# Optimization experiments

Hardware: AMD Instinct MI355X
Metric: run time of the kernel (lower is better)

The kernel has to match this reference:

```python
import jax, jax.numpy as jnp
import numpy as np

SCALE = 0.08838834764831845  # 1/sqrt(128)


def setup_inputs() -> dict:
    key = jax.random.key(0)
    k1, k2, k3, k4 = jax.random.split(key, 4)
    B, Sq, H, D = 1, 2048, 32, 128
    Skv, K = 4096, 256
    return {
        "q": jax.random.normal(k1, (B, Sq, H, D), jnp.float32),
        "kv": jax.random.normal(k2, (B, Skv, 2, D), jnp.float32),  # stacked K,V (MQA)
        "attn_sink": jax.random.normal(k3, (H,), jnp.float32),
        "topk_idxs": jax.random.randint(k4, (B, Sq, K), 0, Skv),
    }


def reference(q, kv, attn_sink, topk_idxs):
    # q:        [B, Sq, H, D]
    # kv:       [B, Skv, 2, D]  (index 0 = keys, 1 = values; shared across heads)
    # topk_idxs:[B, Sq, K]      per-query selected KV positions
    # attn_sink:[H]             per-head sink logit added to the softmax denominator
    B = q.shape[0]
    # Gather selected KV per query: [B, Sq, K, 2, D]
    gathered = kv[jnp.arange(B)[:, None, None], topk_idxs]
    k = gathered[..., 0, :]  # [B, Sq, K, D]
    v = gathered[..., 1, :]  # [B, Sq, K, D]

    scores = jnp.einsum("bqhd,bqkd->bqhk", q, k) * SCALE  # [B, Sq, H, K]
    sink = attn_sink[None, None, :, None]                  # [1, 1, H, 1]

    # Numerically stable softmax over K selected tokens + sink logit.
    m = jnp.maximum(jnp.max(scores, axis=-1, keepdims=True), sink)
    e = jnp.exp(scores - m)
    denom = jnp.sum(e, axis=-1, keepdims=True) + jnp.exp(sink - m)
    probs = e / denom                                      # sink absorbs leftover mass

    out = jnp.einsum("bqhk,bqkd->bqhd", probs, v)          # [B, Sq, H, D]
    return out
```

## Files before the change

kernel.cpp:

```cpp
#include <hip/hip_runtime.h>
#include <hip/hip_bf16.h>

#define SQ 2048
#define NH 32
#define DH 128
#define NK 256
#define SCALE 0.08838834764831845f
#define LOG2E 1.4426950408889634f

typedef __attribute__((ext_vector_type(8))) __bf16 bf16x8;
typedef __attribute__((ext_vector_type(4))) float floatx4;

#define KS_STRIDE 136
#define VB_STRIDE 72
#define PB_STRIDE 264

#define OFF_KV   16896
#define OFF_RED  35328
#define OFF_RED2 35840
#define SMEM_SZ  36352

#define SCHED_PIN() __builtin_amdgcn_sched_barrier(0)

__device__ __forceinline__ unsigned pk_bf16(float a, float b) {
  union { __hip_bfloat162 h2; unsigned u; } c;
  c.h2 = __float22bfloat162_rn(make_float2(a, b));
  return c.u;
}

__device__ __forceinline__ float fast_exp2(float x) {
#if __has_builtin(__builtin_amdgcn_exp2f)
  return __builtin_amdgcn_exp2f(x);
#else
  return exp2f(x);
#endif
}

template <int CTRL>
__device__ __forceinline__ float dpp_rot(float x) {
  int i = __builtin_bit_cast(int, x);
  i = __builtin_amdgcn_mov_dpp(i, CTRL, 0xF, 0xF, true);
  return __builtin_bit_cast(float, i);
}
#define RED16_MAX(v) { v = fmaxf(v, dpp_rot<0x121>(v)); v = fmaxf(v, dpp_rot<0x122>(v)); \
                       v = fmaxf(v, dpp_rot<0x124>(v)); v = fmaxf(v, dpp_rot<0x128>(v)); }
#define RED16_SUM(v) { v += dpp_rot<0x121>(v); v += dpp_rot<0x122>(v); \
                       v += dpp_rot<0x124>(v); v += dpp_rot<0x128>(v); }

__global__ __launch_bounds__(256) void kv_to_bf16(const float* __restrict__ kv,
                                                  unsigned short* __restrict__ kvb) {
  int i = blockIdx.x * 256 + threadIdx.x;
  float4 f = ((const float4*)kv)[i];
  uint2 o = { pk_bf16(f.x, f.y), pk_bf16(f.z, f.w) };
  ((uint2*)kvb)[i] = o;
}

struct KR { uint4 v[4]; };
struct VR { uint4 a, b, c, d; };

__device__ __forceinline__ KR k_load(const unsigned short* __restrict__ kvb,
                                     const int* __restrict__ tkg, int c, int tid) {
  int r = tid >> 2, seg = tid & 3;
  int idx = tkg[c * 64 + r];
  const uint4* p = (const uint4*)(kvb + (size_t)idx * 256 + seg * 32);
  KR k;
#pragma unroll
  for (int i = 0; i < 4; i++) k.v[i] = p[i];
  return k;
}

__device__ __forceinline__ void k_write(unsigned short* kvbuf, const KR& k, int tid) {
  int r = tid >> 2, seg = tid & 3;
  uint4* d = (uint4*)&kvbuf[r * KS_STRIDE + seg * 32];
#pragma unroll
  for (int i = 0; i < 4; i++) d[i] = k.v[i];
}

__device__ __forceinline__ VR v_load(const unsigned short* __restrict__ kvb,
                                     const int* __restrict__ tkg, int c, int tid) {
  int rg = tid & 15, dg = tid >> 4;
  int r0 = rg * 4, d0 = dg * 8;
  int4 i4 = *(const int4*)&tkg[c * 64 + r0];
  VR v;
  v.a = *(const uint4*)(kvb + (size_t)i4.x * 256 + 128 + d0);
  v.b = *(const uint4*)(kvb + (size_t)i4.y * 256 + 128 + d0);
  v.c = *(const uint4*)(kvb + (size_t)i4.z * 256 + 128 + d0);
  v.d = *(const uint4*)(kvb + (size_t)i4.w * 256 + 128 + d0);
  return v;
}

__device__ __forceinline__ void v_write(unsigned short* kvbuf, const VR& v, int tid) {
  int rg = tid & 15, dg = tid >> 4;
  int r0 = rg * 4, d0 = dg * 8;
  const unsigned* pa = (const unsigned*)&v.a;
  const unsigned* pb = (const unsigned*)&v.b;
  const unsigned* pc = (const unsigned*)&v.c;
  const unsigned* pd = (const unsigned*)&v.d;
#pragma unroll
  for (int w = 0; w < 4; w++) {
    unsigned lo01 = __builtin_amdgcn_perm(pb[w], pa[w], 0x05040100u);
    unsigned lo23 = __builtin_amdgcn_perm(pd[w], pc[w], 0x05040100u);
    unsigned hi01 = __builtin_amdgcn_perm(pb[w], pa[w], 0x07060302u);
    unsigned hi23 = __builtin_amdgcn_perm(pd[w], pc[w], 0x07060302u);
    uint2 lo = { lo01, lo23 }, hi = { hi01, hi23 };
    *(uint2*)&kvbuf[(d0 + 2 * w) * VB_STRIDE + r0] = lo;
    *(uint2*)&kvbuf[(d0 + 2 * w + 1) * VB_STRIDE + r0] = hi;
  }
}

__device__ __forceinline__ void gemm1(const unsigned short* kvbuf,
                                      const bf16x8 af[2][4], int nrow, int quad,
                                      floatx4& a0, floatx4& a1) {
  a0 = (floatx4){0.f, 0.f, 0.f, 0.f};
  a1 = (floatx4){0.f, 0.f, 0.f, 0.f};
  __builtin_amdgcn_s_setprio(1);
#pragma unroll
  for (int ks = 0; ks < 4; ks++) {
    bf16x8 b = *(const bf16x8*)&kvbuf[nrow * KS_STRIDE + ks * 32 + quad * 8];
    a0 = __builtin_amdgcn_mfma_f32_16x16x32_bf16(af[0][ks], b, a0, 0, 0, 0);
    a1 = __builtin_amdgcn_mfma_f32_16x16x32_bf16(af[1][ks], b, a1, 0, 0, 0);
  }
  __builtin_amdgcn_s_setprio(0);
}

__device__ __forceinline__ void pv_chunk(const unsigned short* pbuf,
                                         const unsigned short* kvbuf, int c,
                                         int wave, int quad, int l16,
                                         floatx4 oacc[2][2]) {
  __builtin_amdgcn_s_setprio(1);
#pragma unroll
  for (int ks = 0; ks < 2; ks++) {
    int kof = c * 64 + ks * 32 + quad * 8;
    bf16x8 a0 = *(const bf16x8*)&pbuf[l16 * PB_STRIDE + kof];
    bf16x8 a1 = *(const bf16x8*)&pbuf[(16 + l16) * PB_STRIDE + kof];
    int kl = ks * 32 + quad * 8;
    bf16x8 b0 = *(const bf16x8*)&kvbuf[(wave * 32 + l16) * VB_STRIDE + kl];
    bf16x8 b1 = *(const bf16x8*)&kvbuf[(wave * 32 + 16 + l16) * VB_STRIDE + kl];
    oacc[0][0] = __builtin_amdgcn_mfma_f32_16x16x32_bf16(a0, b0, oacc[0][0], 0, 0, 0);
    oacc[0][1] = __builtin_amdgcn_mfma_f32_16x16x32_bf16(a0, b1, oacc[0][1], 0, 0, 0);
    oacc[1][0] = __builtin_amdgcn_mfma_f32_16x16x32_bf16(a1, b0, oacc[1][0], 0, 0, 0);
    oacc[1][1] = __builtin_amdgcn_mfma_f32_16x16x32_bf16(a1, b1, oacc[1][1], 0, 0, 0);
  }
  __builtin_amdgcn_s_setprio(0);
}

__global__ __launch_bounds__(256, 4) void sparse_attn_kernel(
    const float* __restrict__ q, const unsigned short* __restrict__ kvb,
    const float* __restrict__ sink, const int* __restrict__ topk,
    float* __restrict__ out) {
  __shared__ __align__(16) char smem[SMEM_SZ];
  unsigned short* pbuf  = (unsigned short*)smem;
  unsigned short* kvbuf = (unsigned short*)(smem + OFF_KV);
  float* red  = (float*)(smem + OFF_RED);
  float* red2 = (float*)(smem + OFF_RED2);

  const int tid = threadIdx.x;
  const int s = blockIdx.x;
  const int wave = tid >> 6;
  const int lane = tid & 63;
  const int quad = lane >> 4;
  const int l16 = lane & 15;
  const int* tkg = topk + (size_t)s * NK;

  KR k0 = k_load(kvb, tkg, 0, tid);
  SCHED_PIN();

  const float QSC = SCALE * LOG2E;
  const float* qp = q + (size_t)s * (NH * DH);
  float4 qf[2][4][2];
#pragma unroll
  for (int mt = 0; mt < 2; mt++)
#pragma unroll
    for (int ks = 0; ks < 4; ks++) {
      const float* base = qp + (mt * 16 + l16) * DH + ks * 32 + quad * 8;
      qf[mt][ks][0] = ((const float4*)base)[0];
      qf[mt][ks][1] = ((const float4*)base)[1];
    }
  KR k1 = k_load(kvb, tkg, 1, tid);
  KR k2 = k_load(kvb, tkg, 2, tid);
  SCHED_PIN();

  float snk[2][4];
#pragma unroll
  for (int mt = 0; mt < 2; mt++)
#pragma unroll
    for (int r = 0; r < 4; r++)
      snk[mt][r] = sink[mt * 16 + quad * 4 + r] * LOG2E;

  bf16x8 afrag[2][4];
#pragma unroll
  for (int mt = 0; mt < 2; mt++)
#pragma unroll
    for (int ks = 0; ks < 4; ks++) {
      float4 f0 = qf[mt][ks][0], f1 = qf[mt][ks][1];
      uint4 u = { pk_bf16(f0.x * QSC, f0.y * QSC), pk_bf16(f0.z * QSC, f0.w * QSC),
                  pk_bf16(f1.x * QSC, f1.y * QSC), pk_bf16(f1.z * QSC, f1.w * QSC) };
      afrag[mt][ks] = __builtin_bit_cast(bf16x8, u);
    }
  k_write(kvbuf, k0, tid);
  __syncthreads();

  const int nrow = wave * 16 + l16;

  floatx4 sc[4][2];
  gemm1(kvbuf, afrag, nrow, quad, sc[0][0], sc[0][1]);
  __syncthreads();
  k_write(kvbuf, k1, tid);
  KR k3 = k_load(kvb, tkg, 3, tid);
  SCHED_PIN();
  __syncthreads();

  gemm1(kvbuf, afrag, nrow, quad, sc[1][0], sc[1][1]);
  __syncthreads();
  k_write(kvbuf, k2, tid);
  VR v0 = v_load(kvb, tkg, 0, tid);
  SCHED_PIN();
  __syncthreads();

  gemm1(kvbuf, afrag, nrow, quad, sc[2][0], sc[2][1]);
  __syncthreads();
  k_write(kvbuf, k3, tid);
  VR v1 = v_load(kvb, tkg, 1, tid);
  SCHED_PIN();
  __syncthreads();

  gemm1(kvbuf, afrag, nrow, quad, sc[3][0], sc[3][1]);
  __syncthreads();
  v_write(kvbuf, v0, tid);

  float mh[2][4];
#pragma unroll
  for (int mt = 0; mt < 2; mt++)
#pragma unroll
    for (int r = 0; r < 4; r++) {
      float v = fmaxf(fmaxf(sc[0][mt][r], sc[1][mt][r]),
                      fmaxf(sc[2][mt][r], sc[3][mt][r]));
      RED16_MAX(v);
      mh[mt][r] = v;
    }
  if (l16 == 0) {
#pragma unroll
    for (int mt = 0; mt < 2; mt++)
#pragma unroll
      for (int r = 0; r < 4; r++)
        red[wave * 32 + mt * 16 + quad * 4 + r] = mh[mt][r];
  }
  __syncthreads();
  VR v2 = v_load(kvb, tkg, 2, tid);
  SCHED_PIN();
#pragma unroll
  for (int mt = 0; mt < 2; mt++)
#pragma unroll
    for (int r = 0; r < 4; r++) {
      int h = mt * 16 + quad * 4 + r;
      float v = snk[mt][r];
#pragma unroll
      for (int w = 0; w < 4; w++) v = fmaxf(v, red[w * 32 + h]);
      mh[mt][r] = v;
    }
  float ps[2][4];
#pragma unroll
  for (int mt = 0; mt < 2; mt++)
#pragma unroll
    for (int r = 0; r < 4; r++) {
      float acc = 0.f;
#pragma unroll
      for (int c = 0; c < 4; c++) {
        float e = fast_exp2(sc[c][mt][r] - mh[mt][r]);
        sc[c][mt][r] = e;
        acc += e;
      }
      RED16_SUM(acc);
      ps[mt][r] = acc;
    }
  if (l16 == 0) {
#pragma unroll
    for (int mt = 0; mt < 2; mt++)
#pragma unroll
      for (int r = 0; r < 4; r++)
        red2[wave * 32 + mt * 16 + quad * 4 + r] = ps[mt][r];
  }
  __syncthreads();
  float inv[2][4];
#pragma unroll
  for (int mt = 0; mt < 2; mt++)
#pragma unroll
    for (int r = 0; r < 4; r++) {
      float dd = fast_exp2(snk[mt][r] - mh[mt][r]);
#pragma unroll
      for (int w = 0; w < 4; w++) dd += red2[w * 32 + mt * 16 + quad * 4 + r];
      inv[mt][r] = 1.0f / dd;
    }
#pragma unroll
  for (int c = 0; c < 4; c++)
#pragma unroll
    for (int mt = 0; mt < 2; mt++) {
      int col = c * 64 + wave * 16 + l16;
      unsigned short* pb = &pbuf[(mt * 16 + quad * 4) * PB_STRIDE + col];
      unsigned p01 = pk_bf16(sc[c][mt][0], sc[c][mt][1]);
      unsigned p23 = pk_bf16(sc[c][mt][2], sc[c][mt][3]);
      pb[0] = (unsigned short)p01;
      pb[PB_STRIDE] = (unsigned short)(p01 >> 16);
      pb[2 * PB_STRIDE] = (unsigned short)p23;
      pb[3 * PB_STRIDE] = (unsigned short)(p23 >> 16);
    }
  __syncthreads();

  floatx4 oacc[2][2];
#pragma unroll
  for (int mt = 0; mt < 2; mt++)
#pragma unroll
    for (int nt = 0; nt < 2; nt++)
      oacc[mt][nt] = (floatx4){0.f, 0.f, 0.f, 0.f};

  VR v3 = v_load(kvb, tkg, 3, tid);
  SCHED_PIN();
  pv_chunk(pbuf, kvbuf, 0, wave, quad, l16, oacc);
  __syncthreads();
  v_write(kvbuf, v1, tid);
  __syncthreads();

  pv_chunk(pbuf, kvbuf, 1, wave, quad, l16, oacc);
  __syncthreads();
  v_write(kvbuf, v2, tid);
  __syncthreads();

  pv_chunk(pbuf, kvbuf, 2, wave, quad, l16, oacc);
  __syncthreads();
  v_write(kvbuf, v3, tid);
  __syncthreads();

  pv_chunk(pbuf, kvbuf, 3, wave, quad, l16, oacc);

  {
    float* op = out + (size_t)s * (NH * DH);
#pragma unroll
    for (int mt = 0; mt < 2; mt++)
#pragma unroll
      for (int nt = 0; nt < 2; nt++)
#pragma unroll
        for (int r4 = 0; r4 < 4; r4++) {
          int h = mt * 16 + quad * 4 + r4;
          int d = wave * 32 + nt * 16 + l16;
          op[h * DH + d] = oacc[mt][nt][r4] * inv[mt][r4];
        }
  }
}

extern "C" void kernel_launch(void* const* d_in, const int* in_sizes, int n_in,
                              void* d_out, int out_size, void* d_ws, size_t ws_size,
                              hipStream_t stream) {
  (void)in_sizes; (void)n_in; (void)out_size; (void)ws_size;
  const float* q    = (const float*)d_in[0];
  const float* kv   = (const float*)d_in[1];
  const float* sink = (const float*)d_in[2];
  const int*   topk = (const int*)d_in[3];
  float* out = (float*)d_out;
  unsigned short* kvb = (unsigned short*)d_ws;

  kv_to_bf16<<<dim3(1024), dim3(256), 0, stream>>>(kv, kvb);
  sparse_attn_kernel<<<dim3(SQ), dim3(256), 0, stream>>>(q, kvb, sink, topk, out);
}
```

Measured before the change: 129.1 us.

## Split heads across two blocks per query, swizzle LDS, merge softmax reductions

Measured after the change: 166.5 us. 29.0% more time.

```diff
diff --git a/kernel.cpp b/kernel.cpp
--- a/kernel.cpp
+++ b/kernel.cpp
@@ -11,16 +11,14 @@
 typedef __attribute__((ext_vector_type(8))) __bf16 bf16x8;
 typedef __attribute__((ext_vector_type(4))) float floatx4;
 
-#define KS_STRIDE 136
-#define VB_STRIDE 72
-#define PB_STRIDE 264
-
-#define OFF_KV   16896
-#define OFF_RED  35328
-#define OFF_RED2 35840
-#define SMEM_SZ  36352
+#define OFF_KV   8192
+#define OFF_RED  (OFF_KV + 16384)
+#define OFF_RED2 (OFF_RED + 256)
+#define SMEM_SZ  25088
 
 #define SCHED_PIN() __builtin_amdgcn_sched_barrier(0)
+
+__device__ __forceinline__ int swz(int row) { return ((row ^ (row >> 3)) & 7) << 4; }
 
 __device__ __forceinline__ unsigned pk_bf16(float a, float b) {
   union { __hip_bfloat162 h2; unsigned u; } c;
@@ -69,11 +67,13 @@
   return k;
 }
 
-__device__ __forceinline__ void k_write(unsigned short* kvbuf, const KR& k, int tid) {
+__device__ __forceinline__ void k_write(char* kbuf, const KR& k, int tid) {
   int r = tid >> 2, seg = tid & 3;
-  uint4* d = (uint4*)&kvbuf[r * KS_STRIDE + seg * 32];
-#pragma unroll
-  for (int i = 0; i < 4; i++) d[i] = k.v[i];
+  int base = r * 256 + seg * 64;
+  int sw = swz(r);
+#pragma unroll
+  for (int i = 0; i < 4; i++)
+    *(uint4*)(kbuf + ((base + i * 16) ^ sw)) = k.v[i];
 }
 
 __device__ __forceinline__ VR v_load(const unsigned short* __restrict__ kvb,
@@ -89,7 +89,7 @@
   return v;
 }
 
-__device__ __forceinline__ void v_write(unsigned short* kvbuf, const VR& v, int tid) {
+__device__ __forceinline__ void v_write(char* vbuf, const VR& v, int tid) {
   int rg = tid & 15, dg = tid >> 4;
   int r0 = rg * 4, d0 = dg * 8;
   const unsigned* pa = (const unsigned*)&v.a;
@@ -103,247 +103,209 @@
     unsigned hi01 = __builtin_amdgcn_perm(pb[w], pa[w], 0x07060302u);
     unsigned hi23 = __builtin_amdgcn_perm(pd[w], pc[w], 0x07060302u);
     uint2 lo = { lo01, lo23 }, hi = { hi01, hi23 };
-    *(uint2*)&kvbuf[(d0 + 2 * w) * VB_STRIDE + r0] = lo;
-    *(uint2*)&kvbuf[(d0 + 2 * w + 1) * VB_STRIDE + r0] = hi;
-  }
-}
-
-__device__ __forceinline__ void gemm1(const unsigned short* kvbuf,
-                                      const bf16x8 af[2][4], int nrow, int quad,
-                                      floatx4& a0, floatx4& a1) {
-  a0 = (floatx4){0.f, 0.f, 0.f, 0.f};
-  a1 = (floatx4){0.f, 0.f, 0.f, 0.f};
+    int ra = d0 + 2 * w, rb = ra + 1;
+    *(uint2*)(vbuf + ((ra * 128 + r0 * 2) ^ swz(ra))) = lo;
+    *(uint2*)(vbuf + ((rb * 128 + r0 * 2) ^ swz(rb))) = hi;
+  }
+}
+
+__device__ __forceinline__ void gemm1(const char* kbuf, const bf16x8 af[4],
+                                      int nrow, int quad, floatx4& acc) {
+  acc = (floatx4){0.f, 0.f, 0.f, 0.f};
+  int sw = swz(nrow);
   __builtin_amdgcn_s_setprio(1);
 #pragma unroll
   for (int ks = 0; ks < 4; ks++) {
-    bf16x8 b = *(const bf16x8*)&kvbuf[nrow * KS_STRIDE + ks * 32 + quad * 8];
-    a0 = __builtin_amdgcn_mfma_f32_16x16x32_bf16(af[0][ks], b, a0, 0, 0, 0);
-    a1 = __builtin_amdgcn_mfma_f32_16x16x32_bf16(af[1][ks], b, a1, 0, 0, 0);
+    bf16x8 b = *(const bf16x8*)(kbuf + ((nrow * 256 + ks * 64 + quad * 16) ^ sw));
+    acc = __builtin_amdgcn_mfma_f32_16x16x32_bf16(af[ks], b, acc, 0, 0, 0);
   }
   __builtin_amdgcn_s_setprio(0);
 }
 
-__device__ __forceinline__ void pv_chunk(const unsigned short* pbuf,
-                                         const unsigned short* kvbuf, int c,
+__device__ __forceinline__ void pv_chunk(const char* pbuf, const char* vbuf, int c,
                                          int wave, int quad, int l16,
-                                         floatx4 oacc[2][2]) {
+                                         floatx4 oacc[2]) {
   __builtin_amdgcn_s_setprio(1);
 #pragma unroll
   for (int ks = 0; ks < 2; ks++) {
-    int kof = c * 64 + ks * 32 + quad * 8;
-    bf16x8 a0 = *(const bf16x8*)&pbuf[l16 * PB_STRIDE + kof];
-    bf16x8 a1 = *(const bf16x8*)&pbuf[(16 + l16) * PB_STRIDE + kof];
-    int kl = ks * 32 + quad * 8;
-    bf16x8 b0 = *(const bf16x8*)&kvbuf[(wave * 32 + l16) * VB_STRIDE + kl];
-    bf16x8 b1 = *(const bf16x8*)&kvbuf[(wave * 32 + 16 + l16) * VB_STRIDE + kl];
-    oacc[0][0] = __builtin_amdgcn_mfma_f32_16x16x32_bf16(a0, b0, oacc[0][0], 0, 0, 0);
-    oacc[0][1] = __builtin_amdgcn_mfma_f32_16x16x32_bf16(a0, b1, oacc[0][1], 0, 0, 0);
-    oacc[1][0] = __builtin_amdgcn_mfma_f32_16x16x32_bf16(a1, b0, oacc[1][0], 0, 0, 0);
-    oacc[1][1] = __builtin_amdgcn_mfma_f32_16x16x32_bf16(a1, b1, oacc[1][1], 0, 0, 0);
+    int kof = (c * 64 + ks * 32 + quad * 8) * 2;
+    bf16x8 a = *(const bf16x8*)(pbuf + ((l16 * 512 + kof) ^ swz(l16)));
+    int kl = (ks * 32 + quad * 8) * 2;
+    int r0 = wave * 32 + l16, r1 = r0 + 16;
+    bf16x8 b0 = *(const bf16x8*)(vbuf + ((r0 * 128 + kl) ^ swz(r0)));
+    bf16x8 b1 = *(const bf16x8*)(vbuf + ((r1 * 128 + kl) ^ swz(r1)));
+    oacc[0] = __builtin_amdgcn_mfma_f32_16x16x32_bf16(a, b0, oacc[0], 0, 0, 0);
+    oacc[1] = __builtin_amdgcn_mfma_f32_16x16x32_bf16(a, b1, oacc[1], 0, 0, 0);
   }
   __builtin_amdgcn_s_setprio(0);
 }
 
-__global__ __launch_bounds__(256, 4) void sparse_attn_kernel(
+__global__ __launch_bounds__(256, 5) void sparse_attn_kernel(
     const float* __restrict__ q, const unsigned short* __restrict__ kvb,
     const float* __restrict__ sink, const int* __restrict__ topk,
     float* __restrict__ out) {
   __shared__ __align__(16) char smem[SMEM_SZ];
-  unsigned short* pbuf  = (unsigned short*)smem;
-  unsigned short* kvbuf = (unsigned short*)(smem + OFF_KV);
+  char* pbuf  = smem;
+  char* kvbuf = smem + OFF_KV;
   float* red  = (float*)(smem + OFF_RED);
   float* red2 = (float*)(smem + OFF_RED2);
 
   const int tid = threadIdx.x;
-  const int s = blockIdx.x;
+  const int s = blockIdx.x >> 1;
+  const int h0 = (blockIdx.x & 1) * 16;
   const int wave = tid >> 6;
   const int lane = tid & 63;
   const int quad = lane >> 4;
   const int l16 = lane & 15;
   const int* tkg = topk + (size_t)s * NK;
 
-  KR k0 = k_load(kvb, tkg, 0, tid);
-  SCHED_PIN();
+  {
+    int r = tid >> 2, seg = tid & 3;
+    int idx = tkg[r];
+    const uint4* p = (const uint4*)(kvb + (size_t)idx * 256 + seg * 32);
+    uint4 t0 = p[0], t1 = p[1], t2 = p[2], t3 = p[3];
+    int base = r * 256 + seg * 64, sw = swz(r);
+    *(uint4*)(kvbuf + ((base) ^ sw)) = t0;
+    *(uint4*)(kvbuf + ((base + 16) ^ sw)) = t1;
+    *(uint4*)(kvbuf + ((base + 32) ^ sw)) = t2;
+    *(uint4*)(kvbuf + ((base + 48) ^ sw)) = t3;
+  }
+  KR k1 = k_load(kvb, tkg, 1, tid);
+  SCHED_PIN();
+
+  float snk[4];
+#pragma unroll
+  for (int r = 0; r < 4; r++)
+    snk[r] = sink[h0 + quad * 4 + r] * LOG2E;
 
   const float QSC = SCALE * LOG2E;
-  const float* qp = q + (size_t)s * (NH * DH);
-  float4 qf[2][4][2];
-#pragma unroll
-  for (int mt = 0; mt < 2; mt++)
-#pragma unroll
-    for (int ks = 0; ks < 4; ks++) {
-      const float* base = qp + (mt * 16 + l16) * DH + ks * 32 + quad * 8;
-      qf[mt][ks][0] = ((const float4*)base)[0];
-      qf[mt][ks][1] = ((const float4*)base)[1];
+  const float* qrow = q + (size_t)s * (NH * DH) + (h0 + l16) * DH;
+  bf16x8 afrag[4];
+#pragma unroll
+  for (int ks = 0; ks < 4; ks++) {
+    const float* base = qrow + ks * 32 + quad * 8;
+    float4 f0 = ((const float4*)base)[0];
+    float4 f1 = ((const float4*)base)[1];
+    uint4 u = { pk_bf16(f0.x * QSC, f0.y * QSC), pk_bf16(f0.z * QSC, f0.w * QSC),
+                pk_bf16(f1.x * QSC, f1.y * QSC), pk_bf16(f1.z * QSC, f1.w * QSC) };
+    afrag[ks] = __builtin_bit_cast(bf16x8, u);
+  }
+  __syncthreads();
+
+  const int nrow = wave * 16 + l16;
+
+  floatx4 sc[4];
+  KR k2 = k_load(kvb, tkg, 2, tid);
+  SCHED_PIN();
+  gemm1(kvbuf, afrag, nrow, quad, sc[0]);
+  __syncthreads();
+  k_write(kvbuf, k1, tid);
+  __syncthreads();
+  KR k3 = k_load(kvb, tkg, 3, tid);
+  SCHED_PIN();
+  gemm1(kvbuf, afrag, nrow, quad, sc[1]);
+  __syncthreads();
+  k_write(kvbuf, k2, tid);
+  __syncthreads();
+  VR v0 = v_load(kvb, tkg, 0, tid);
+  SCHED_PIN();
+  gemm1(kvbuf, afrag, nrow, quad, sc[2]);
+  __syncthreads();
+  k_write(kvbuf, k3, tid);
+  __syncthreads();
+  VR v1 = v_load(kvb, tkg, 1, tid);
+  SCHED_PIN();
+  gemm1(kvbuf, afrag, nrow, quad, sc[3]);
+
+  float mh[4], ps[4];
+#pragma unroll
+  for (int r = 0; r < 4; r++) {
+    float v = fmaxf(fmaxf(sc[0][r], sc[1][r]), fmaxf(sc[2][r], sc[3][r]));
+    RED16_MAX(v);
+    mh[r] = v;
+  }
+#pragma unroll
+  for (int r = 0; r < 4; r++) {
+    float acc = 0.f;
+#pragma unroll
+    for (int c = 0; c < 4; c++) {
+      float e = fast_exp2(sc[c][r] - mh[r]);
+      sc[c][r] = e;
+      acc += e;
     }
-  KR k1 = k_load(kvb, tkg, 1, tid);
-  KR k2 = k_load(kvb, tkg, 2, tid);
-  SCHED_PIN();
-
-  float snk[2][4];
-#pragma unroll
-  for (int mt = 0; mt < 2; mt++)
-#pragma unroll
-    for (int r = 0; r < 4; r++)
-      snk[mt][r] = sink[mt * 16 + quad * 4 + r] * LOG2E;
-
-  bf16x8 afrag[2][4];
-#pragma unroll
-  for (int mt = 0; mt < 2; mt++)
-#pragma unroll
-    for (int ks = 0; ks < 4; ks++) {
-      float4 f0 = qf[mt][ks][0], f1 = qf[mt][ks][1];
-      uint4 u = { pk_bf16(f0.x * QSC, f0.y * QSC), pk_bf16(f0.z * QSC, f0.w * QSC),
-                  pk_bf16(f1.x * QSC, f1.y * QSC), pk_bf16(f1.z * QSC, f1.w * QSC) };
-      afrag[mt][ks] = __builtin_bit_cast(bf16x8, u);
+    RED16_SUM(acc);
+    ps[r] = acc;
+  }
+  if (l16 == 0) {
+#pragma unroll
+    for (int r = 0; r < 4; r++) {
+      red[wave * 16 + quad * 4 + r]  = mh[r];
+      red2[wave * 16 + quad * 4 + r] = ps[r];
     }
-  k_write(kvbuf, k0, tid);
-  __syncthreads();
-
-  const int nrow = wave * 16 + l16;
-
-  floatx4 sc[4][2];
-  gemm1(kvbuf, afrag, nrow, quad, sc[0][0], sc[0][1]);
-  __syncthreads();
-  k_write(kvbuf, k1, tid);
-  KR k3 = k_load(kvb, tkg, 3, tid);
-  SCHED_PIN();
-  __syncthreads();
-
-  gemm1(kvbuf, afrag, nrow, quad, sc[1][0], sc[1][1]);
-  __syncthreads();
-  k_write(kvbuf, k2, tid);
-  VR v0 = v_load(kvb, tkg, 0, tid);
-  SCHED_PIN();
-  __syncthreads();
-
-  gemm1(kvbuf, afrag, nrow, quad, sc[2][0], sc[2][1]);
-  __syncthreads();
-  k_write(kvbuf, k3, tid);
-  VR v1 = v_load(kvb, tkg, 1, tid);
-  SCHED_PIN();
-  __syncthreads();
-
-  gemm1(kvbuf, afrag, nrow, quad, sc[3][0], sc[3][1]);
+  }
   __syncthreads();
   v_write(kvbuf, v0, tid);
-
-  float mh[2][4];
-#pragma unroll
-  for (int mt = 0; mt < 2; mt++)
-#pragma unroll
-    for (int r = 0; r < 4; r++) {
-      float v = fmaxf(fmaxf(sc[0][mt][r], sc[1][mt][r]),
-                      fmaxf(sc[2][mt][r], sc[3][mt][r]));
-      RED16_MAX(v);
-      mh[mt][r] = v;
+  VR v2 = v_load(kvb, tkg, 2, tid);
+  SCHED_PIN();
+  float inv[4], sf[4];
+#pragma unroll
+  for (int r = 0; r < 4; r++) {
+    int h = quad * 4 + r;
+    float M = snk[r];
+#pragma unroll
+    for (int w = 0; w < 4; w++) M = fmaxf(M, red[w * 16 + h]);
+    float dd = fast_exp2(snk[r] - M);
+#pragma unroll
+    for (int w = 0; w < 4; w++)
+      dd += red2[w * 16 + h] * fast_exp2(red[w * 16 + h] - M);
+    inv[r] = 1.0f / dd;
+    sf[r] = fast_exp2(mh[r] - M);
+  }
+#pragma unroll
+  for (int c = 0; c < 4; c++) {
+    int col = c * 64 + wave * 16 + l16;
+    unsigned p01 = pk_bf16(sc[c][0] * sf[0], sc[c][1] * sf[1]);
+    unsigned p23 = pk_bf16(sc[c][2] * sf[2], sc[c][3] * sf[3]);
+    unsigned short vals[4] = { (unsigned short)p01, (unsigned short)(p01 >> 16),
+                               (unsigned short)p23, (unsigned short)(p23 >> 16) };
+#pragma unroll
+    for (int j = 0; j < 4; j++) {
+      int h = quad * 4 + j;
+      *(unsigned short*)(pbuf + ((h * 512 + col * 2) ^ swz(h))) = vals[j];
     }
-  if (l16 == 0) {
-#pragma unroll
-    for (int mt = 0; mt < 2; mt++)
-#pragma unroll
-      for (int r = 0; r < 4; r++)
-        red[wave * 32 + mt * 16 + quad * 4 + r] = mh[mt][r];
-  }
-  __syncthreads();
-  VR v2 = v_load(kvb, tkg, 2, tid);
-  SCHED_PIN();
-#pragma unroll
-  for (int mt = 0; mt < 2; mt++)
-#pragma unroll
-    for (int r = 0; r < 4; r++) {
-      int h = mt * 16 + quad * 4 + r;
-      float v = snk[mt][r];
-#pragma unroll
-      for (int w = 0; w < 4; w++) v = fmaxf(v, red[w * 32 + h]);
-      mh[mt][r] = v;
-    }
-  float ps[2][4];
-#pragma unroll
-  for (int mt = 0; mt < 2; mt++)
-#pragma unroll
-    for (int r = 0; r < 4; r++) {
-      float acc = 0.f;
-#pragma unroll
-      for (int c = 0; c < 4; c++) {
-        float e = fast_exp2(sc[c][mt][r] - mh[mt][r]);
-        sc[c][mt][r] = e;
-        acc += e;
+  }
+  __syncthreads();
+
+  floatx4 oacc[2];
+  oacc[0] = (floatx4){0.f, 0.f, 0.f, 0.f};
+  oacc[1] = (floatx4){0.f, 0.f, 0.f, 0.f};
+
+  VR v3 = v_load(kvb, tkg, 3, tid);
+  SCHED_PIN();
+  pv_chunk(pbuf, kvbuf, 0, wave, quad, l16, oacc);
+  __syncthreads();
+  v_write(kvbuf, v1, tid);
+  __syncthreads();
+  pv_chunk(pbuf, kvbuf, 1, wave, quad, l16, oacc);
+  __syncthreads();
+  v_write(kvbuf, v2, tid);
+  __syncthreads();
+  pv_chunk(pbuf, kvbuf, 2, wave, quad, l16, oacc);
+  __syncthreads();
+  v_write(kvbuf, v3, tid);
+  __syncthreads();
+  pv_chunk(pbuf, kvbuf, 3, wave, quad, l16, oacc);
+
+  {
+    float* op = out + (size_t)s * (NH * DH) + h0 * DH;
+#pragma unroll
+    for (int nt = 0; nt < 2; nt++)
+#pragma unroll
+      for (int r4 = 0; r4 < 4; r4++) {
+        int h = quad * 4 + r4;
+        int d = wave * 32 + nt * 16 + l16;
+        op[h * DH + d] = oacc[nt][r4] * inv[r4];
       }
-      RED16_SUM(acc);
-      ps[mt][r] = acc;
-    }
-  if (l16 == 0) {
-#pragma unroll
-    for (int mt = 0; mt < 2; mt++)
-#pragma unroll
-      for (int r = 0; r < 4; r++)
-        red2[wave * 32 + mt * 16 + quad * 4 + r] = ps[mt][r];
-  }
-  __syncthreads();
-  float inv[2][4];
-#pragma unroll
-  for (int mt = 0; mt < 2; mt++)
-#pragma unroll
-    for (int r = 0; r < 4; r++) {
-      float dd = fast_exp2(snk[mt][r] - mh[mt][r]);
-#pragma unroll
-      for (int w = 0; w < 4; w++) dd += red2[w * 32 + mt * 16 + quad * 4 + r];
-      inv[mt][r] = 1.0f / dd;
-    }
-#pragma unroll
-  for (int c = 0; c < 4; c++)
-#pragma unroll
-    for (int mt = 0; mt < 2; mt++) {
-      int col = c * 64 + wave * 16 + l16;
-      unsigned short* pb = &pbuf[(mt * 16 + quad * 4) * PB_STRIDE + col];
-      unsigned p01 = pk_bf16(sc[c][mt][0], sc[c][mt][1]);
-      unsigned p23 = pk_bf16(sc[c][mt][2], sc[c][mt][3]);
-      pb[0] = (unsigned short)p01;
-      pb[PB_STRIDE] = (unsigned short)(p01 >> 16);
-      pb[2 * PB_STRIDE] = (unsigned short)p23;
-      pb[3 * PB_STRIDE] = (unsigned short)(p23 >> 16);
-    }
-  __syncthreads();
-
-  floatx4 oacc[2][2];
-#pragma unroll
-  for (int mt = 0; mt < 2; mt++)
-#pragma unroll
-    for (int nt = 0; nt < 2; nt++)
-      oacc[mt][nt] = (floatx4){0.f, 0.f, 0.f, 0.f};
-
-  VR v3 = v_load(kvb, tkg, 3, tid);
-  SCHED_PIN();
-  pv_chunk(pbuf, kvbuf, 0, wave, quad, l16, oacc);
-  __syncthreads();
-  v_write(kvbuf, v1, tid);
-  __syncthreads();
-
-  pv_chunk(pbuf, kvbuf, 1, wave, quad, l16, oacc);
-  __syncthreads();
-  v_write(kvbuf, v2, tid);
-  __syncthreads();
-
-  pv_chunk(pbuf, kvbuf, 2, wave, quad, l16, oacc);
-  __syncthreads();
-  v_write(kvbuf, v3, tid);
-  __syncthreads();
-
-  pv_chunk(pbuf, kvbuf, 3, wave, quad, l16, oacc);
-
-  {
-    float* op = out + (size_t)s * (NH * DH);
-#pragma unroll
-    for (int mt = 0; mt < 2; mt++)
-#pragma unroll
-      for (int nt = 0; nt < 2; nt++)
-#pragma unroll
-        for (int r4 = 0; r4 < 4; r4++) {
-          int h = mt * 16 + quad * 4 + r4;
-          int d = wave * 32 + nt * 16 + l16;
-          op[h * DH + d] = oacc[mt][nt][r4] * inv[mt][r4];
-        }
   }
 }
 
@@ -359,5 +321,5 @@
   unsigned short* kvb = (unsigned short*)d_ws;
 
   kv_to_bf16<<<dim3(1024), dim3(256), 0, stream>>>(kv, kvb);
-  sparse_attn_kernel<<<dim3(SQ), dim3(256), 0, stream>>>(q, kvb, sink, topk, out);
-}
+  sparse_attn_kernel<<<dim3(SQ * 2), dim3(256), 0, stream>>>(q, kvb, sink, topk, out);
+}
```

## Swizzle LDS layouts, merge softmax reductions into one barrier, shorten prefetch depth

Applied to the files above, without the earlier changes.

After: 124.9 us. -3.2%, faster.

```diff
diff --git a/kernel.cpp b/kernel.cpp
--- a/kernel.cpp
+++ b/kernel.cpp
@@ -11,16 +11,14 @@
 typedef __attribute__((ext_vector_type(8))) __bf16 bf16x8;
 typedef __attribute__((ext_vector_type(4))) float floatx4;
 
-#define KS_STRIDE 136
-#define VB_STRIDE 72
-#define PB_STRIDE 264
-
-#define OFF_KV   16896
-#define OFF_RED  35328
-#define OFF_RED2 35840
-#define SMEM_SZ  36352
+#define OFF_KV   16384
+#define OFF_RED  32768
+#define OFF_RED2 33280
+#define SMEM_SZ  33792
 
 #define SCHED_PIN() __builtin_amdgcn_sched_barrier(0)
+
+__device__ __forceinline__ int swz(int row) { return ((row ^ (row >> 3)) & 7) << 4; }
 
 __device__ __forceinline__ unsigned pk_bf16(float a, float b) {
   union { __hip_bfloat162 h2; unsigned u; } c;
@@ -60,20 +58,22 @@
 
 __device__ __forceinline__ KR k_load(const unsigned short* __restrict__ kvb,
                                      const int* __restrict__ tkg, int c, int tid) {
-  int r = tid >> 2, seg = tid & 3;
+  int r = tid >> 2, c4 = tid & 3;
   int idx = tkg[c * 64 + r];
-  const uint4* p = (const uint4*)(kvb + (size_t)idx * 256 + seg * 32);
+  const char* p = (const char*)(kvb + (size_t)idx * 256);
   KR k;
 #pragma unroll
-  for (int i = 0; i < 4; i++) k.v[i] = p[i];
+  for (int i = 0; i < 4; i++)
+    k.v[i] = *(const uint4*)(p + i * 64 + c4 * 16);
   return k;
 }
 
-__device__ __forceinline__ void k_write(unsigned short* kvbuf, const KR& k, int tid) {
-  int r = tid >> 2, seg = tid & 3;
-  uint4* d = (uint4*)&kvbuf[r * KS_STRIDE + seg * 32];
-#pragma unroll
-  for (int i = 0; i < 4; i++) d[i] = k.v[i];
+__device__ __forceinline__ void k_write(char* kbuf, const KR& k, int tid) {
+  int r = tid >> 2, c4 = tid & 3;
+  int sw = swz(r);
+#pragma unroll
+  for (int i = 0; i < 4; i++)
+    *(uint4*)(kbuf + ((r * 256 + i * 64 + c4 * 16) ^ sw)) = k.v[i];
 }
 
 __device__ __forceinline__ VR v_load(const unsigned short* __restrict__ kvb,
@@ -89,7 +89,7 @@
   return v;
 }
 
-__device__ __forceinline__ void v_write(unsigned short* kvbuf, const VR& v, int tid) {
+__device__ __forceinline__ void v_write(char* vbuf, const VR& v, int tid) {
   int rg = tid & 15, dg = tid >> 4;
   int r0 = rg * 4, d0 = dg * 8;
   const unsigned* pa = (const unsigned*)&v.a;
@@ -103,39 +103,40 @@
     unsigned hi01 = __builtin_amdgcn_perm(pb[w], pa[w], 0x07060302u);
     unsigned hi23 = __builtin_amdgcn_perm(pd[w], pc[w], 0x07060302u);
     uint2 lo = { lo01, lo23 }, hi = { hi01, hi23 };
-    *(uint2*)&kvbuf[(d0 + 2 * w) * VB_STRIDE + r0] = lo;
-    *(uint2*)&kvbuf[(d0 + 2 * w + 1) * VB_STRIDE + r0] = hi;
-  }
-}
-
-__device__ __forceinline__ void gemm1(const unsigned short* kvbuf,
-                                      const bf16x8 af[2][4], int nrow, int quad,
-                                      floatx4& a0, floatx4& a1) {
+    int ra = d0 + 2 * w, rb = ra + 1;
+    *(uint2*)(vbuf + ((ra * 128 + r0 * 2) ^ swz(ra))) = lo;
+    *(uint2*)(vbuf + ((rb * 128 + r0 * 2) ^ swz(rb))) = hi;
+  }
+}
+
+__device__ __forceinline__ void gemm1(const char* kbuf, const bf16x8 af[2][4],
+                                      int nrow, int quad, floatx4& a0, floatx4& a1) {
   a0 = (floatx4){0.f, 0.f, 0.f, 0.f};
   a1 = (floatx4){0.f, 0.f, 0.f, 0.f};
+  int sw = swz(nrow);
   __builtin_amdgcn_s_setprio(1);
 #pragma unroll
   for (int ks = 0; ks < 4; ks++) {
-    bf16x8 b = *(const bf16x8*)&kvbuf[nrow * KS_STRIDE + ks * 32 + quad * 8];
+    bf16x8 b = *(const bf16x8*)(kbuf + ((nrow * 256 + ks * 64 + quad * 16) ^ sw));
     a0 = __builtin_amdgcn_mfma_f32_16x16x32_bf16(af[0][ks], b, a0, 0, 0, 0);
     a1 = __builtin_amdgcn_mfma_f32_16x16x32_bf16(af[1][ks], b, a1, 0, 0, 0);
   }
   __builtin_amdgcn_s_setprio(0);
 }
 
-__device__ __forceinline__ void pv_chunk(const unsigned short* pbuf,
-                                         const unsigned short* kvbuf, int c,
+__device__ __forceinline__ void pv_chunk(const char* pbuf, const char* vbuf, int c,
                                          int wave, int quad, int l16,
                                          floatx4 oacc[2][2]) {
   __builtin_amdgcn_s_setprio(1);
 #pragma unroll
   for (int ks = 0; ks < 2; ks++) {
-    int kof = c * 64 + ks * 32 + quad * 8;
-    bf16x8 a0 = *(const bf16x8*)&pbuf[l16 * PB_STRIDE + kof];
-    bf16x8 a1 = *(const bf16x8*)&pbuf[(16 + l16) * PB_STRIDE + kof];
-    int kl = ks * 32 + quad * 8;
-    bf16x8 b0 = *(const bf16x8*)&kvbuf[(wave * 32 + l16) * VB_STRIDE + kl];
-    bf16x8 b1 = *(const bf16x8*)&kvbuf[(wave * 32 + 16 + l16) * VB_STRIDE + kl];
+    int kof = (c * 64 + ks * 32 + quad * 8) * 2;
+    bf16x8 a0 = *(const bf16x8*)(pbuf + ((l16 * 512 + kof) ^ swz(l16)));
+    bf16x8 a1 = *(const bf16x8*)(pbuf + (((16 + l16) * 512 + kof) ^ swz(16 + l16)));
+    int kl = (ks * 32 + quad * 8) * 2;
+    int r0 = wave * 32 + l16, r1 = r0 + 16;
+    bf16x8 b0 = *(const bf16x8*)(vbuf + ((r0 * 128 + kl) ^ swz(r0)));
+    bf16x8 b1 = *(const bf16x8*)(vbuf + ((r1 * 128 + kl) ^ swz(r1)));
     oacc[0][0] = __builtin_amdgcn_mfma_f32_16x16x32_bf16(a0, b0, oacc[0][0], 0, 0, 0);
     oacc[0][1] = __builtin_amdgcn_mfma_f32_16x16x32_bf16(a0, b1, oacc[0][1], 0, 0, 0);
     oacc[1][0] = __builtin_amdgcn_mfma_f32_16x16x32_bf16(a1, b0, oacc[1][0], 0, 0, 0);
@@ -149,8 +150,8 @@
     const float* __restrict__ sink, const int* __restrict__ topk,
     float* __restrict__ out) {
   __shared__ __align__(16) char smem[SMEM_SZ];
-  unsigned short* pbuf  = (unsigned short*)smem;
-  unsigned short* kvbuf = (unsigned short*)(smem + OFF_KV);
+  char* pbuf  = smem;
+  char* kvbuf = smem + OFF_KV;
   float* red  = (float*)(smem + OFF_RED);
   float* red2 = (float*)(smem + OFF_RED2);
 
@@ -162,42 +163,46 @@
   const int l16 = lane & 15;
   const int* tkg = topk + (size_t)s * NK;
 
-  KR k0 = k_load(kvb, tkg, 0, tid);
-  SCHED_PIN();
+  {
+    int r = tid >> 2, c4 = tid & 3;
+    int idx = tkg[r];
+    const char* p = (const char*)(kvb + (size_t)idx * 256);
+    uint4 t0 = *(const uint4*)(p + 0 * 64 + c4 * 16);
+    uint4 t1 = *(const uint4*)(p + 1 * 64 + c4 * 16);
+    uint4 t2 = *(const uint4*)(p + 2 * 64 + c4 * 16);
+    uint4 t3 = *(const uint4*)(p + 3 * 64 + c4 * 16);
+    int sw = swz(r);
+    *(uint4*)(kvbuf + ((r * 256 + 0 * 64 + c4 * 16) ^ sw)) = t0;
+    *(uint4*)(kvbuf + ((r * 256 + 1 * 64 + c4 * 16) ^ sw)) = t1;
+    *(uint4*)(kvbuf + ((r * 256 + 2 * 64 + c4 * 16) ^ sw)) = t2;
+    *(uint4*)(kvbuf + ((r * 256 + 3 * 64 + c4 * 16) ^ sw)) = t3;
+  }
+  KR k1 = k_load(kvb, tkg, 1, tid);
+  SCHED_PIN();
+
+  float snk[2][4];
+#pragma unroll
+  for (int mt = 0; mt < 2; mt++)
+#pragma unroll
+    for (int r = 0; r < 4; r++)
+      snk[mt][r] = sink[mt * 16 + quad * 4 + r] * LOG2E;
 
   const float QSC = SCALE * LOG2E;
   const float* qp = q + (size_t)s * (NH * DH);
-  float4 qf[2][4][2];
-#pragma unroll
-  for (int mt = 0; mt < 2; mt++)
+  bf16x8 afrag[2][4];
+#pragma unroll
+  for (int mt = 0; mt < 2; mt++) {
+    const float* qrow = qp + (mt * 16 + l16) * DH;
 #pragma unroll
     for (int ks = 0; ks < 4; ks++) {
-      const float* base = qp + (mt * 16 + l16) * DH + ks * 32 + quad * 8;
-      qf[mt][ks][0] = ((const float4*)base)[0];
-      qf[mt][ks][1] = ((const float4*)base)[1];
-    }
-  KR k1 = k_load(kvb, tkg, 1, tid);
-  KR k2 = k_load(kvb, tkg, 2, tid);
-  SCHED_PIN();
-
-  float snk[2][4];
-#pragma unroll
-  for (int mt = 0; mt < 2; mt++)
-#pragma unroll
-    for (int r = 0; r < 4; r++)
-      snk[mt][r] = sink[mt * 16 + quad * 4 + r] * LOG2E;
-
-  bf16x8 afrag[2][4];
-#pragma unroll
-  for (int mt = 0; mt < 2; mt++)
-#pragma unroll
-    for (int ks = 0; ks < 4; ks++) {
-      float4 f0 = qf[mt][ks][0], f1 = qf[mt][ks][1];
+      const float* base = qrow + ks * 32 + quad * 8;
+      float4 f0 = ((const float4*)base)[0];
+      float4 f1 = ((const float4*)base)[1];
       uint4 u = { pk_bf16(f0.x * QSC, f0.y * QSC), pk_bf16(f0.z * QSC, f0.w * QSC),
                   pk_bf16(f1.x * QSC, f1.y * QSC), pk_bf16(f1.z * QSC, f1.w * QSC) };
       afrag[mt][ks] = __builtin_bit_cast(bf16x8, u);
     }
-  k_write(kvbuf, k0, tid);
+  }
   __syncthreads();
 
   const int nrow = wave * 16 + l16;
@@ -206,29 +211,27 @@
   gemm1(kvbuf, afrag, nrow, quad, sc[0][0], sc[0][1]);
   __syncthreads();
   k_write(kvbuf, k1, tid);
+  KR k2 = k_load(kvb, tkg, 2, tid);
+  SCHED_PIN();
+  __syncthreads();
+
+  gemm1(kvbuf, afrag, nrow, quad, sc[1][0], sc[1][1]);
+  __syncthreads();
+  k_write(kvbuf, k2, tid);
   KR k3 = k_load(kvb, tkg, 3, tid);
   SCHED_PIN();
   __syncthreads();
 
-  gemm1(kvbuf, afrag, nrow, quad, sc[1][0], sc[1][1]);
-  __syncthreads();
-  k_write(kvbuf, k2, tid);
+  gemm1(kvbuf, afrag, nrow, quad, sc[2][0], sc[2][1]);
+  __syncthreads();
+  k_write(kvbuf, k3, tid);
   VR v0 = v_load(kvb, tkg, 0, tid);
   SCHED_PIN();
   __syncthreads();
 
-  gemm1(kvbuf, afrag, nrow, quad, sc[2][0], sc[2][1]);
-  __syncthreads();
-  k_write(kvbuf, k3, tid);
-  VR v1 = v_load(kvb, tkg, 1, tid);
-  SCHED_PIN();
-  __syncthreads();
-
   gemm1(kvbuf, afrag, nrow, quad, sc[3][0], sc[3][1]);
-  __syncthreads();
-  v_write(kvbuf, v0, tid);
-
-  float mh[2][4];
+
+  float mh[2][4], ps[2][4];
 #pragma unroll
   for (int mt = 0; mt < 2; mt++)
 #pragma unroll
@@ -238,27 +241,6 @@
       RED16_MAX(v);
       mh[mt][r] = v;
     }
-  if (l16 == 0) {
-#pragma unroll
-    for (int mt = 0; mt < 2; mt++)
-#pragma unroll
-      for (int r = 0; r < 4; r++)
-        red[wave * 32 + mt * 16 + quad * 4 + r] = mh[mt][r];
-  }
-  __syncthreads();
-  VR v2 = v_load(kvb, tkg, 2, tid);
-  SCHED_PIN();
-#pragma unroll
-  for (int mt = 0; mt < 2; mt++)
-#pragma unroll
-    for (int r = 0; r < 4; r++) {
-      int h = mt * 16 + quad * 4 + r;
-      float v = snk[mt][r];
-#pragma unroll
-      for (int w = 0; w < 4; w++) v = fmaxf(v, red[w * 32 + h]);
-      mh[mt][r] = v;
-    }
-  float ps[2][4];
 #pragma unroll
   for (int mt = 0; mt < 2; mt++)
 #pragma unroll
@@ -277,32 +259,45 @@
 #pragma unroll
     for (int mt = 0; mt < 2; mt++)
 #pragma unroll
-      for (int r = 0; r < 4; r++)
+      for (int r = 0; r < 4; r++) {
+        red[wave * 32 + mt * 16 + quad * 4 + r]  = mh[mt][r];
         red2[wave * 32 + mt * 16 + quad * 4 + r] = ps[mt][r];
-  }
-  __syncthreads();
-  float inv[2][4];
+      }
+  }
+  __syncthreads();
+  v_write(kvbuf, v0, tid);
+  VR v1 = v_load(kvb, tkg, 1, tid);
+  SCHED_PIN();
+  float inv[2][4], sf[2][4];
 #pragma unroll
   for (int mt = 0; mt < 2; mt++)
 #pragma unroll
     for (int r = 0; r < 4; r++) {
-      float dd = fast_exp2(snk[mt][r] - mh[mt][r]);
-#pragma unroll
-      for (int w = 0; w < 4; w++) dd += red2[w * 32 + mt * 16 + quad * 4 + r];
+      int h = mt * 16 + quad * 4 + r;
+      float M = snk[mt][r];
+#pragma unroll
+      for (int w = 0; w < 4; w++) M = fmaxf(M, red[w * 32 + h]);
+      float dd = fast_exp2(snk[mt][r] - M);
+#pragma unroll
+      for (int w = 0; w < 4; w++)
+        dd += red2[w * 32 + h] * fast_exp2(red[w * 32 + h] - M);
       inv[mt][r] = 1.0f / dd;
+      sf[mt][r] = fast_exp2(mh[mt][r] - M);
     }
 #pragma unroll
   for (int c = 0; c < 4; c++)
 #pragma unroll
     for (int mt = 0; mt < 2; mt++) {
       int col = c * 64 + wave * 16 + l16;
-      unsigned short* pb = &pbuf[(mt * 16 + quad * 4) * PB_STRIDE + col];
-      unsigned p01 = pk_bf16(sc[c][mt][0], sc[c][mt][1]);
-      unsigned p23 = pk_bf16(sc[c][mt][2], sc[c][mt][3]);
-      pb[0] = (unsigned short)p01;
-      pb[PB_STRIDE] = (unsigned short)(p01 >> 16);
-      pb[2 * PB_STRIDE] = (unsigned short)p23;
-      pb[3 * PB_STRIDE] = (unsigned short)(p23 >> 16);
+      unsigned p01 = pk_bf16(sc[c][mt][0] * sf[mt][0], sc[c][mt][1] * sf[mt][1]);
+      unsigned p23 = pk_bf16(sc[c][mt][2] * sf[mt][2], sc[c][mt][3] * sf[mt][3]);
+      unsigned short vals[4] = { (unsigned short)p01, (unsigned short)(p01 >> 16),
+                                 (unsigned short)p23, (unsigned short)(p23 >> 16) };
+#pragma unroll
+      for (int j = 0; j < 4; j++) {
+        int h = mt * 16 + quad * 4 + j;
+        *(unsigned short*)(pbuf + ((h * 512 + col * 2) ^ swz(h))) = vals[j];
+      }
     }
   __syncthreads();
 
@@ -313,16 +308,18 @@
     for (int nt = 0; nt < 2; nt++)
       oacc[mt][nt] = (floatx4){0.f, 0.f, 0.f, 0.f};
 
+  pv_chunk(pbuf, kvbuf, 0, wave, quad, l16, oacc);
+  __syncthreads();
+  v_write(kvbuf, v1, tid);
+  VR v2 = v_load(kvb, tkg, 2, tid);
+  SCHED_PIN();
+  __syncthreads();
+
+  pv_chunk(pbuf, kvbuf, 1, wave, quad, l16, oacc);
+  __syncthreads();
+  v_write(kvbuf, v2, tid);
   VR v3 = v_load(kvb, tkg, 3, tid);
   SCHED_PIN();
-  pv_chunk(pbuf, kvbuf, 0, wave, quad, l16, oacc);
-  __syncthreads();
-  v_write(kvbuf, v1, tid);
-  __syncthreads();
-
-  pv_chunk(pbuf, kvbuf, 1, wave, quad, l16, oacc);
-  __syncthreads();
-  v_write(kvbuf, v2, tid);
   __syncthreads();
 
   pv_chunk(pbuf, kvbuf, 2, wave, quad, l16, oacc);
```
